# Kernel tuning notes

Hardware: AMD Instinct MI355X
Metric: run time of the kernel (lower is better)

Reference implementation:

```python
import jax, jax.numpy as jnp
import numpy as np

FORWARD_W = 1.0
BACKWARD_W = 1.0
NORMAL_W = 0.1
EPS = 1e-6


def setup_inputs() -> dict:
    key = jax.random.key(0)
    ks = jax.random.split(key, 5)
    N, M = 8192, 8192
    sp = jax.random.normal(ks[0], (N, 3), dtype=jnp.float32)
    tp = jax.random.normal(ks[1], (M, 3), dtype=jnp.float32)
    sn = jax.random.normal(ks[2], (N, 3), dtype=jnp.float32)
    tn = jax.random.normal(ks[3], (M, 3), dtype=jnp.float32)
    sn = sn / jnp.linalg.norm(sn, axis=1, keepdims=True)
    tn = tn / jnp.linalg.norm(tn, axis=1, keepdims=True)
    rot6d = jnp.array([1.0, 0.05, -0.02, 0.03, 1.0, 0.04], dtype=jnp.float32)
    rot6d = rot6d + 0.01 * jax.random.normal(ks[4], (6,), dtype=jnp.float32)
    return {
        'source_points': sp, 'target_points': tp,
        'source_normals': sn, 'target_normals': tn,
        'translation': jnp.zeros(3, jnp.float32),
        'rotation_6d': rot6d,
        'scale': jnp.ones(3, jnp.float32),
    }


def rotation_6d_to_matrix(r6):
    a1, a2 = r6[:3], r6[3:]
    b1 = a1 / jnp.linalg.norm(a1)
    b2 = a2 - jnp.sum(b1 * a2) * b1
    b2 = b2 / jnp.linalg.norm(b2)
    b3 = jnp.cross(b1, b2)
    return jnp.stack([b1, b2, b3], axis=1)  # (3,3), columns are b1,b2,b3


def cos_sim(a, b):
    na = jnp.maximum(jnp.linalg.norm(a, axis=1), EPS)
    nb = jnp.maximum(jnp.linalg.norm(b, axis=1), EPS)
    return jnp.sum(a * b, axis=1) / (na * nb)


def reference(source_points, target_points, source_normals, target_normals,
              translation, rotation_6d, scale):
    R = rotation_6d_to_matrix(rotation_6d)
    # apply_transformation: scale -> rotate -> translate
    src = (source_points * scale[None, :]) @ R.T + translation[None, :]  # (N,3)
    src_n = source_normals @ R.T  # (N,3)

    # pairwise squared distances (N,M)
    d2 = (jnp.sum(src * src, axis=1)[:, None]
          + jnp.sum(target_points * target_points, axis=1)[None, :]
          - 2.0 * src @ target_points.T)
    d2 = jnp.maximum(d2, 0.0)

    d_s2t = jnp.min(d2, axis=1)          # (N,) squared NN dist source->target
    idx_s = jnp.argmin(d2, axis=1)       # (N,)
    d_t2s = jnp.min(d2, axis=0)          # (M,)
    idx_t = jnp.argmin(d2, axis=0)       # (M,)

    loss = FORWARD_W * jnp.mean(d_s2t) + BACKWARD_W * jnp.mean(d_t2s)

    # normal loss: 1 - |cos| against matched normals (both directions)
    cn_s = 1.0 - jnp.abs(cos_sim(src_n, target_normals[idx_s]))
    cn_t = 1.0 - jnp.abs(cos_sim(target_normals, src_n[idx_t]))
    loss = loss + NORMAL_W * (jnp.mean(cn_s) + jnp.mean(cn_t))
    return loss
```

## Files before the change

### kernel.cpp

```cpp
#include <hip/hip_runtime.h>
#include <math.h>

#define FW 1.0f
#define BW 1.0f
#define NW 0.1f
#define EPSV 1e-6f

#define BT  256
#define MPT 4
#define JCH 256

#define COMPUTE_R(r6)                                                         \
    float a1x = (r6)[0], a1y = (r6)[1], a1z = (r6)[2];                        \
    float a2x = (r6)[3], a2y = (r6)[4], a2z = (r6)[5];                        \
    float n1 = sqrtf(a1x*a1x + a1y*a1y + a1z*a1z);                            \
    float b1x = a1x/n1, b1y = a1y/n1, b1z = a1z/n1;                           \
    float dp = b1x*a2x + b1y*a2y + b1z*a2z;                                   \
    float u2x = a2x - dp*b1x, u2y = a2y - dp*b1y, u2z = a2z - dp*b1z;         \
    float n2 = sqrtf(u2x*u2x + u2y*u2y + u2z*u2z);                            \
    float b2x = u2x/n2, b2y = u2y/n2, b2z = u2z/n2;                           \
    float b3x = b1y*b2z - b1z*b2y;                                            \
    float b3y = b1z*b2x - b1x*b2z;                                            \
    float b3z = b1x*b2y - b1y*b2x;

__global__ __launch_bounds__(BT) void transform_kernel(
    const float* __restrict__ sp, const float* __restrict__ tp,
    const float* __restrict__ sn,
    const float* __restrict__ trans, const float* __restrict__ r6,
    const float* __restrict__ scl,
    float4* __restrict__ src4, float4* __restrict__ tgt4,
    float4* __restrict__ srcn4,
    unsigned long long* __restrict__ min_s,
    unsigned long long* __restrict__ min_t,
    float* __restrict__ out, int N, int M)
{
    int i = blockIdx.x * BT + threadIdx.x;

    if (blockIdx.y == 1) {
        if (i < M) {
            float x = tp[3*i], y = tp[3*i+1], z = tp[3*i+2];
            tgt4[i] = make_float4(x, y, z, x*x + y*y + z*z);
            min_t[i] = ~0ull;
        }
        return;
    }

    if (i == 0) out[0] = 0.f;
    if (i >= N) return;
    min_s[i] = ~0ull;

    COMPUTE_R(r6)

    float qx = sp[3*i]   * scl[0];
    float qy = sp[3*i+1] * scl[1];
    float qz = sp[3*i+2] * scl[2];
    float sx = b1x*qx + b2x*qy + b3x*qz + trans[0];
    float sy = b1y*qx + b2y*qy + b3y*qz + trans[1];
    float sz = b1z*qx + b2z*qy + b3z*qz + trans[2];
    src4[i] = make_float4(sx, sy, sz, sx*sx + sy*sy + sz*sz);

    float nx = sn[3*i], ny = sn[3*i+1], nz = sn[3*i+2];
    srcn4[i] = make_float4(b1x*nx + b2x*ny + b3x*nz,
                           b1y*nx + b2y*ny + b3y*nz,
                           b1z*nx + b2z*ny + b3z*nz, 0.f);
}

__global__ __launch_bounds__(BT) void min_kernel(
    const float4* __restrict__ src4, const float4* __restrict__ tgt4,
    unsigned long long* __restrict__ min_s,
    unsigned long long* __restrict__ min_t, int N, int M)
{
    const float4* A; const float4* B; unsigned long long* outm; int nA, nB;
    if (blockIdx.z == 0) { A = src4; B = tgt4; outm = min_s; nA = N; nB = M; }
    else                 { A = tgt4; B = src4; outm = min_t; nA = M; nB = N; }

    __shared__ float4 bs[JCH];
    const int tid   = threadIdx.x;
    const int aBase = blockIdx.x * (BT * MPT);
    const int jBase = blockIdx.y * JCH;

    float cx[MPT], cy[MPT], cz[MPT], s2[MPT], best[MPT];
    int bj[MPT];
    #pragma unroll
    for (int p = 0; p < MPT; p++) {
        int ia = aBase + p*BT + tid;
        float4 a = A[ia < nA ? ia : 0];
        cx[p] = -2.f*a.x; cy[p] = -2.f*a.y; cz[p] = -2.f*a.z;
        s2[p] = a.w;
        best[p] = 3.4e38f; bj[p] = 0;
    }
    {
        int jb = jBase + tid;
        bs[tid] = B[jb < nB ? jb : nB - 1];
    }
    __syncthreads();

    int jLim = nB - jBase; if (jLim > JCH) jLim = JCH;
    if (jLim == JCH) {
        #pragma unroll 4
        for (int j = 0; j < JCH; j++) {
            float4 b = bs[j];
            #pragma unroll
            for (int p = 0; p < MPT; p++) {
                float e = fmaf(cz[p], b.z, b.w);
                e = fmaf(cy[p], b.y, e);
                e = fmaf(cx[p], b.x, e);
                bool c = e < best[p];
                best[p] = c ? e : best[p];
                bj[p]   = c ? j : bj[p];
            }
        }
    } else {
        for (int j = 0; j < jLim; j++) {
            float4 b = bs[j];
            #pragma unroll
            for (int p = 0; p < MPT; p++) {
                float e = fmaf(cz[p], b.z, b.w);
                e = fmaf(cy[p], b.y, e);
                e = fmaf(cx[p], b.x, e);
                bool c = e < best[p];
                best[p] = c ? e : best[p];
                bj[p]   = c ? j : bj[p];
            }
        }
    }

    #pragma unroll
    for (int p = 0; p < MPT; p++) {
        int ia = aBase + p*BT + tid;
        if (ia < nA) {
            float d = fmaxf(best[p] + s2[p], 0.f);
            unsigned long long pk =
                ((unsigned long long)__float_as_uint(d) << 32) |
                (unsigned int)(jBase + bj[p]);
            atomicMin(&outm[ia], pk);
        }
    }
}

__global__ __launch_bounds__(BT) void reduce_kernel(
    const unsigned long long* __restrict__ min_s,
    const unsigned long long* __restrict__ min_t,
    const float4* __restrict__ srcn4, const float* __restrict__ tn,
    float* __restrict__ out, int N, int M)
{
    int gid = blockIdx.x * BT + threadIdx.x;
    float contrib = 0.f;

    if (gid < N) {
        unsigned long long pk = min_s[gid];
        float d = __uint_as_float((unsigned int)(pk >> 32));
        int idx = (int)(unsigned int)(pk & 0xffffffffull);
        float4 nv = srcn4[gid];
        float tx = tn[3*idx], ty = tn[3*idx+1], tz = tn[3*idx+2];
        float na = fmaxf(sqrtf(nv.x*nv.x + nv.y*nv.y + nv.z*nv.z), EPSV);
        float nb = fmaxf(sqrtf(tx*tx + ty*ty + tz*tz), EPSV);
        float cs = (nv.x*tx + nv.y*ty + nv.z*tz) / (na * nb);
        contrib = (FW * d + NW * (1.f - fabsf(cs))) * (1.f / N);
    } else if (gid < N + M) {
        int j = gid - N;
        unsigned long long pk = min_t[j];
        float d = __uint_as_float((unsigned int)(pk >> 32));
        int idx = (int)(unsigned int)(pk & 0xffffffffull);
        float tx = tn[3*j], ty = tn[3*j+1], tz = tn[3*j+2];
        float4 nv = srcn4[idx];
        float na = fmaxf(sqrtf(tx*tx + ty*ty + tz*tz), EPSV);
        float nb = fmaxf(sqrtf(nv.x*nv.x + nv.y*nv.y + nv.z*nv.z), EPSV);
        float cs = (tx*nv.x + ty*nv.y + tz*nv.z) / (na * nb);
        contrib = (BW * d + NW * (1.f - fabsf(cs))) * (1.f / M);
    }

    #pragma unroll
    for (int o = 32; o > 0; o >>= 1)
        contrib += __shfl_down(contrib, o, 64);

    __shared__ float wsum[BT/64];
    if ((threadIdx.x & 63) == 0) wsum[threadIdx.x >> 6] = contrib;
    __syncthreads();
    if (threadIdx.x == 0) {
        float s = 0.f;
        #pragma unroll
        for (int w = 0; w < BT/64; w++) s += wsum[w];
        atomicAdd(out, s);
    }
}

extern "C" void kernel_launch(void* const* d_in, const int* in_sizes, int n_in,
                              void* d_out, int out_size, void* d_ws, size_t ws_size,
                              hipStream_t stream) {
    const float* sp    = (const float*)d_in[0];
    const float* tp    = (const float*)d_in[1];
    const float* sn    = (const float*)d_in[2];
    const float* tn    = (const float*)d_in[3];
    const float* trans = (const float*)d_in[4];
    const float* r6    = (const float*)d_in[5];
    const float* scl   = (const float*)d_in[6];
    float* out = (float*)d_out;

    const int N = in_sizes[0] / 3;
    const int M = in_sizes[1] / 3;

    char* ws = (char*)d_ws;
    float4* src4  = (float4*)(ws);
    float4* tgt4  = (float4*)(ws + (size_t)16*N);
    float4* srcn4 = (float4*)(ws + (size_t)16*N + (size_t)16*M);
    unsigned long long* min_s =
        (unsigned long long*)(ws + (size_t)32*N + (size_t)16*M);
    unsigned long long* min_t = min_s + N;

    int nmax = N > M ? N : M;
    dim3 tgrid((nmax + BT - 1) / BT, 2);
    transform_kernel<<<tgrid, BT, 0, stream>>>(sp, tp, sn, trans, r6, scl,
                                               src4, tgt4, srcn4,
                                               min_s, min_t, out, N, M);

    dim3 mgrid((N + BT*MPT - 1) / (BT*MPT), (M + JCH - 1) / JCH, 2);
    min_kernel<<<mgrid, BT, 0, stream>>>(src4, tgt4, min_s, min_t, N, M);

    int rblocks = (N + M + BT - 1) / BT;
    reduce_kernel<<<rblocks, BT, 0, stream>>>(min_s, min_t, srcn4, tn, out, N, M);
}
```

Measured before the change: 92.69 us.

## Use packed FP32 FMAs in NN min kernel with more points per thread

Measured after the change: 95.41 us. +2.9%, slower.

```diff
diff --git a/kernel.cpp b/kernel.cpp
--- a/kernel.cpp
+++ b/kernel.cpp
@@ -7,8 +7,11 @@
 #define EPSV 1e-6f
 
 #define BT  256
-#define MPT 4
-#define JCH 256
+#define MPT 8
+#define QP  (MPT/2)
+#define JCH 128
+
+typedef float f32x2 __attribute__((ext_vector_type(2)));
 
 #define COMPUTE_R(r6)                                                         \
     float a1x = (r6)[0], a1y = (r6)[1], a1z = (r6)[2];                        \
@@ -74,54 +77,54 @@
     if (blockIdx.z == 0) { A = src4; B = tgt4; outm = min_s; nA = N; nB = M; }
     else                 { A = tgt4; B = src4; outm = min_t; nA = M; nB = N; }
 
-    __shared__ float4 bs[JCH];
     const int tid   = threadIdx.x;
     const int aBase = blockIdx.x * (BT * MPT);
     const int jBase = blockIdx.y * JCH;
-
-    float cx[MPT], cy[MPT], cz[MPT], s2[MPT], best[MPT];
+    if (aBase >= nA || jBase >= nB) return;
+
+    __shared__ float4 bs[JCH];
+
+    f32x2 cx[QP], cy[QP], cz[QP];
+    float s2[MPT], best[MPT];
     int bj[MPT];
     #pragma unroll
-    for (int p = 0; p < MPT; p++) {
-        int ia = aBase + p*BT + tid;
-        float4 a = A[ia < nA ? ia : 0];
-        cx[p] = -2.f*a.x; cy[p] = -2.f*a.y; cz[p] = -2.f*a.z;
-        s2[p] = a.w;
-        best[p] = 3.4e38f; bj[p] = 0;
-    }
-    {
+    for (int q = 0; q < QP; q++) {
+        int i0 = aBase + (2*q  )*BT + tid; if (i0 >= nA) i0 = 0;
+        int i1 = aBase + (2*q+1)*BT + tid; if (i1 >= nA) i1 = 0;
+        float4 a0 = A[i0];
+        float4 a1 = A[i1];
+        cx[q] = (f32x2){-2.f*a0.x, -2.f*a1.x};
+        cy[q] = (f32x2){-2.f*a0.y, -2.f*a1.y};
+        cz[q] = (f32x2){-2.f*a0.z, -2.f*a1.z};
+        s2[2*q] = a0.w; s2[2*q+1] = a1.w;
+        best[2*q] = 3.4e38f; best[2*q+1] = 3.4e38f;
+        bj[2*q] = 0; bj[2*q+1] = 0;
+    }
+    if (tid < JCH) {
         int jb = jBase + tid;
         bs[tid] = B[jb < nB ? jb : nB - 1];
     }
     __syncthreads();
 
     int jLim = nB - jBase; if (jLim > JCH) jLim = JCH;
-    if (jLim == JCH) {
-        #pragma unroll 4
-        for (int j = 0; j < JCH; j++) {
-            float4 b = bs[j];
-            #pragma unroll
-            for (int p = 0; p < MPT; p++) {
-                float e = fmaf(cz[p], b.z, b.w);
-                e = fmaf(cy[p], b.y, e);
-                e = fmaf(cx[p], b.x, e);
-                bool c = e < best[p];
-                best[p] = c ? e : best[p];
-                bj[p]   = c ? j : bj[p];
-            }
-        }
-    } else {
-        for (int j = 0; j < jLim; j++) {
-            float4 b = bs[j];
-            #pragma unroll
-            for (int p = 0; p < MPT; p++) {
-                float e = fmaf(cz[p], b.z, b.w);
-                e = fmaf(cy[p], b.y, e);
-                e = fmaf(cx[p], b.x, e);
-                bool c = e < best[p];
-                best[p] = c ? e : best[p];
-                bj[p]   = c ? j : bj[p];
-            }
+    #pragma unroll 2
+    for (int j = 0; j < jLim; j++) {
+        float4 b = bs[j];
+        f32x2 bx = (f32x2){b.x, b.x};
+        f32x2 by = (f32x2){b.y, b.y};
+        f32x2 bz = (f32x2){b.z, b.z};
+        f32x2 bw = (f32x2){b.w, b.w};
+        #pragma unroll
+        for (int q = 0; q < QP; q++) {
+            f32x2 e = __builtin_elementwise_fma(cz[q], bz, bw);
+            e = __builtin_elementwise_fma(cy[q], by, e);
+            e = __builtin_elementwise_fma(cx[q], bx, e);
+            bool c0 = e.x < best[2*q];
+            best[2*q]   = c0 ? e.x : best[2*q];
+            bj[2*q]     = c0 ? j   : bj[2*q];
+            bool c1 = e.y < best[2*q+1];
+            best[2*q+1] = c1 ? e.y : best[2*q+1];
+            bj[2*q+1]   = c1 ? j   : bj[2*q+1];
         }
     }
 
@@ -214,7 +217,7 @@
                                                src4, tgt4, srcn4,
                                                min_s, min_t, out, N, M);
 
-    dim3 mgrid((N + BT*MPT - 1) / (BT*MPT), (M + JCH - 1) / JCH, 2);
+    dim3 mgrid((nmax + BT*MPT - 1) / (BT*MPT), (nmax + JCH - 1) / JCH, 2);
     min_kernel<<<mgrid, BT, 0, stream>>>(src4, tgt4, min_s, min_t, N, M);
 
     int rblocks = (N + M + BT - 1) / BT;
```

## Pack argmin index into float mantissa low bits and retile min kernel

Applied to the files above, without the earlier changes.

Result: faster. 89.77 us, median of 2 (-3.2%).

```diff
diff --git a/kernel.cpp b/kernel.cpp
--- a/kernel.cpp
+++ b/kernel.cpp
@@ -7,8 +7,8 @@
 #define EPSV 1e-6f
 
 #define BT  256
-#define MPT 4
-#define JCH 256
+#define MPT 8
+#define JCH 128
 
 #define COMPUTE_R(r6)                                                         \
     float a1x = (r6)[0], a1y = (r6)[1], a1z = (r6)[2];                        \
@@ -74,54 +74,40 @@
     if (blockIdx.z == 0) { A = src4; B = tgt4; outm = min_s; nA = N; nB = M; }
     else                 { A = tgt4; B = src4; outm = min_t; nA = M; nB = N; }
 
-    __shared__ float4 bs[JCH];
     const int tid   = threadIdx.x;
     const int aBase = blockIdx.x * (BT * MPT);
     const int jBase = blockIdx.y * JCH;
+    if (aBase >= nA || jBase >= nB) return;
+
+    __shared__ float4 bs[JCH];
 
     float cx[MPT], cy[MPT], cz[MPT], s2[MPT], best[MPT];
-    int bj[MPT];
     #pragma unroll
     for (int p = 0; p < MPT; p++) {
-        int ia = aBase + p*BT + tid;
-        float4 a = A[ia < nA ? ia : 0];
+        int ia = aBase + p*BT + tid; if (ia >= nA) ia = 0;
+        float4 a = A[ia];
         cx[p] = -2.f*a.x; cy[p] = -2.f*a.y; cz[p] = -2.f*a.z;
         s2[p] = a.w;
-        best[p] = 3.4e38f; bj[p] = 0;
-    }
-    {
+        best[p] = 3.4e38f;
+    }
+    if (tid < JCH) {
         int jb = jBase + tid;
         bs[tid] = B[jb < nB ? jb : nB - 1];
     }
     __syncthreads();
 
     int jLim = nB - jBase; if (jLim > JCH) jLim = JCH;
-    if (jLim == JCH) {
-        #pragma unroll 4
-        for (int j = 0; j < JCH; j++) {
-            float4 b = bs[j];
-            #pragma unroll
-            for (int p = 0; p < MPT; p++) {
-                float e = fmaf(cz[p], b.z, b.w);
-                e = fmaf(cy[p], b.y, e);
-                e = fmaf(cx[p], b.x, e);
-                bool c = e < best[p];
-                best[p] = c ? e : best[p];
-                bj[p]   = c ? j : bj[p];
-            }
-        }
-    } else {
-        for (int j = 0; j < jLim; j++) {
-            float4 b = bs[j];
-            #pragma unroll
-            for (int p = 0; p < MPT; p++) {
-                float e = fmaf(cz[p], b.z, b.w);
-                e = fmaf(cy[p], b.y, e);
-                e = fmaf(cx[p], b.x, e);
-                bool c = e < best[p];
-                best[p] = c ? e : best[p];
-                bj[p]   = c ? j : bj[p];
-            }
+    #pragma unroll 2
+    for (int j = 0; j < jLim; j++) {
+        float4 b = bs[j];
+        #pragma unroll
+        for (int p = 0; p < MPT; p++) {
+            float e = fmaf(cz[p], b.z, b.w);
+            e = fmaf(cy[p], b.y, e);
+            e = fmaf(cx[p], b.x, e);
+            float em = __uint_as_float(
+                (__float_as_uint(e) & 0xFFFFFF00u) | (unsigned int)j);
+            best[p] = fminf(best[p], em);
         }
     }
 
@@ -129,10 +115,13 @@
     for (int p = 0; p < MPT; p++) {
         int ia = aBase + p*BT + tid;
         if (ia < nA) {
-            float d = fmaxf(best[p] + s2[p], 0.f);
+            unsigned int eb = __float_as_uint(best[p]);
+            int jloc = (int)(eb & 0xFFu);
+            float ec = __uint_as_float(eb & 0xFFFFFF00u);
+            float d = fmaxf(ec + s2[p], 0.f);
             unsigned long long pk =
                 ((unsigned long long)__float_as_uint(d) << 32) |
-                (unsigned int)(jBase + bj[p]);
+                (unsigned int)(jBase + jloc);
             atomicMin(&outm[ia], pk);
         }
     }
@@ -214,7 +203,7 @@
                                                src4, tgt4, srcn4,
                                                min_s, min_t, out, N, M);
 
-    dim3 mgrid((N + BT*MPT - 1) / (BT*MPT), (M + JCH - 1) / JCH, 2);
+    dim3 mgrid((nmax + BT*MPT - 1) / (BT*MPT), (nmax + JCH - 1) / JCH, 2);
     min_kernel<<<mgrid, BT, 0, stream>>>(src4, tgt4, min_s, min_t, N, M);
 
     int rblocks = (N + M + BT - 1) / BT;
```
